# Kernel tuning notes

Hardware: AMD Instinct MI355X
Metric: run time of the kernel (lower is better)

## Reference

```python
import jax, jax.numpy as jnp
import numpy as np

N = 2048
E = 32768
H = 128
EDGE_FEAT_DIM = 4


def _mlp(x, w1, b1, w2, b2):
    return jax.nn.relu(x @ w1 + b1) @ w2 + b2


def setup_inputs() -> dict:
    key = jax.random.key(0)
    ks = jax.random.split(key, 20)
    s = 0.02
    inp = {
        "mu": jax.random.normal(ks[0], (N, H), jnp.float32),
        "sigma": jax.random.uniform(ks[1], (N, H), jnp.float32),
        "edge_index": jax.random.randint(ks[2], (2, E), 0, N, jnp.int32),
        "edge_dist": jax.random.uniform(ks[3], (E, 1), jnp.float32),
        "edge_conf": jax.random.uniform(ks[4], (E, 1), jnp.float32),
        "edge_angle": jax.random.normal(ks[5], (E, 1), jnp.float32),
        "edge_depth_diff": jax.random.normal(ks[6], (E, 1), jnp.float32),
        # msg_mlp: (2H+4 -> H -> H)
        "msg_w1": jax.random.normal(ks[7], (2 * H + EDGE_FEAT_DIM, H), jnp.float32) * s,
        "msg_b1": jnp.zeros((H,), jnp.float32),
        "msg_w2": jax.random.normal(ks[8], (H, H), jnp.float32) * s,
        "msg_b2": jnp.zeros((H,), jnp.float32),
        # mu_update_mlp: (H -> H -> H)
        "mu_w1": jax.random.normal(ks[9], (H, H), jnp.float32) * s,
        "mu_b1": jnp.zeros((H,), jnp.float32),
        "mu_w2": jax.random.normal(ks[10], (H, H), jnp.float32) * s,
        "mu_b2": jnp.zeros((H,), jnp.float32),
        # sigma_update_mlp: (H+1 -> H -> H)
        "sig_w1": jax.random.normal(ks[11], (H + 1, H), jnp.float32) * s,
        "sig_b1": jnp.zeros((H,), jnp.float32),
        "sig_w2": jax.random.normal(ks[12], (H, H), jnp.float32) * s,
        "sig_b2": jnp.zeros((H,), jnp.float32),
    }
    return inp


def _residuals(edge_index, edge_dist, num_nodes):
    src, dst = edge_index[0], edge_index[1]
    d_AC = edge_dist[:, 0]                                  # (E,)
    adj = jnp.full((num_nodes, num_nodes), -1.0, edge_dist.dtype)
    adj = adj.at[src, dst].set(d_AC)                        # (N, N)
    d_AB = adj[src]                                         # (E, N): d(A, B)
    d_BC_T = adj[:, dst].T                                  # (E, N): d(B, C)
    valid = (d_AB >= 0) & (d_BC_T >= 0)
    two_hop = jnp.where(valid, d_AB + d_BC_T, 0.0)
    path_count = valid.sum(axis=1).astype(edge_dist.dtype)  # (E,)
    mean_two_hop = jnp.where(
        path_count > 0,
        two_hop.sum(axis=1) / jnp.maximum(path_count, 1.0),
        d_AC,
    )
    return jnp.abs(d_AC - mean_two_hop)[:, None]            # (E, 1)


def reference(mu, sigma, edge_index, edge_dist, edge_conf, edge_angle,
              edge_depth_diff, msg_w1, msg_b1, msg_w2, msg_b2,
              mu_w1, mu_b1, mu_w2, mu_b2, sig_w1, sig_b1, sig_w2, sig_b2):
    n = mu.shape[0]
    src, dst = edge_index[0], edge_index[1]
    residuals = _residuals(edge_index, edge_dist, n)        # (E, 1)
    weights = jnp.exp(-residuals)                           # (E, 1)
    edge_feat = jnp.concatenate([edge_dist, edge_conf, edge_angle, edge_depth_diff], axis=-1)
    msg_input = jnp.concatenate([mu[src], sigma[src], edge_feat], axis=-1)
    messages = _mlp(msg_input, msg_w1, msg_b1, msg_w2, msg_b2)  # (E, H)
    weighted_msgs = messages * weights
    agg_msg = jax.ops.segment_sum(weighted_msgs, dst, num_segments=n)
    weight_sum = jax.ops.segment_sum(weights, dst, num_segments=n)
    agg_msg = agg_msg / jnp.maximum(weight_sum, 1e-8)
    mu_new = mu + _mlp(agg_msg, mu_w1, mu_b1, mu_w2, mu_b2)
    # scatter-mean of residuals over incoming edges
    r_sum = jax.ops.segment_sum(residuals, dst, num_segments=n)
    cnt = jax.ops.segment_sum(jnp.ones((residuals.shape[0], 1), residuals.dtype), dst, num_segments=n)
    mean_incoming_r = r_sum / jnp.maximum(cnt, 1.0)
    sigma_input = jnp.concatenate([agg_msg, mean_incoming_r], axis=-1)
    sigma_new = jax.nn.softplus(_mlp(sigma_input, sig_w1, sig_b1, sig_w2, sig_b2))
    return mu_new, sigma_new, residuals
```

## Files before the change

kernel.cpp:

```cpp
#include <hip/hip_runtime.h>
#include <math.h>

#define NNODE 2048
#define NEDGE 32768
#define HID   128
#define NMAT  (NNODE * NNODE)
#define EB    64

__global__ __launch_bounds__(256) void init_kernel(int4* __restrict__ adj4,
                                                   int* __restrict__ deg_src,
                                                   int* __restrict__ deg_dst) {
    int gid = blockIdx.x * 256 + threadIdx.x;
    adj4[gid] = make_int4(-1, -1, -1, -1);
    if (gid < NNODE) { deg_src[gid] = 0; deg_dst[gid] = 0; }
}

__global__ __launch_bounds__(256) void scatter_kernel(const int* __restrict__ ei,
                                                      int* __restrict__ adj_idx,
                                                      int* __restrict__ deg_src,
                                                      int* __restrict__ deg_dst) {
    int e = blockIdx.x * 256 + threadIdx.x;
    if (e < NEDGE) {
        int s = ei[e];
        int d = ei[NEDGE + e];
        atomicMax(&adj_idx[(size_t)s * NNODE + d], e);
        atomicAdd(&deg_src[s], 1);
        atomicAdd(&deg_dst[d], 1);
    }
}

__global__ __launch_bounds__(256) void scan_kernel(const int* __restrict__ deg_src,
                                                   const int* __restrict__ deg_dst,
                                                   int* __restrict__ off_src,
                                                   int* __restrict__ off_dst,
                                                   int* __restrict__ cur_src,
                                                   int* __restrict__ cur_dst) {
    __shared__ int part[256];
    int t = threadIdx.x;
    for (int which = 0; which < 2; ++which) {
        const int* deg = which ? deg_dst : deg_src;
        int* off = which ? off_dst : off_src;
        int* cur = which ? cur_dst : cur_src;
        __syncthreads();
        int base = t * 8;
        int local[8];
        int s = 0;
        #pragma unroll
        for (int i = 0; i < 8; ++i) { local[i] = deg[base + i]; s += local[i]; }
        part[t] = s;
        __syncthreads();
        if (t == 0) {
            int run = 0;
            for (int i = 0; i < 256; ++i) { int v = part[i]; part[i] = run; run += v; }
        }
        __syncthreads();
        int run = part[t];
        #pragma unroll
        for (int i = 0; i < 8; ++i) {
            off[base + i] = run;
            cur[base + i] = run;
            run += local[i];
        }
        if (t == 255) off[NNODE] = run;
    }
}

__global__ __launch_bounds__(256) void fill_kernel(const int* __restrict__ ei,
                                                   int* __restrict__ cur_src,
                                                   int* __restrict__ cur_dst,
                                                   int* __restrict__ list_src,
                                                   int* __restrict__ list_dst) {
    int e = blockIdx.x * 256 + threadIdx.x;
    if (e < NEDGE) {
        int s = ei[e];
        int d = ei[NEDGE + e];
        int p1 = atomicAdd(&cur_src[s], 1);
        list_src[p1] = e;
        int p2 = atomicAdd(&cur_dst[d], 1);
        list_dst[p2] = e;
    }
}

__global__ __launch_bounds__(256) void residual_kernel(const int* __restrict__ ei,
                                                       const float* __restrict__ dist,
                                                       const int* __restrict__ adj_idx,
                                                       const int* __restrict__ off_src,
                                                       const int* __restrict__ list_src,
                                                       float* __restrict__ res_out,
                                                       float* __restrict__ wbuf) {
    int grp = threadIdx.x >> 4;
    int lane = threadIdx.x & 15;
    int e = blockIdx.x * 16 + grp;
    int A = ei[e];
    int C = ei[NEDGE + e];
    int beg = off_src[A];
    int end = off_src[A + 1];
    float sum = 0.0f, cnt = 0.0f;
    for (int i = beg + lane; i < end; i += 16) {
        int ep = list_src[i];
        int B = ei[NEDGE + ep];
        if (adj_idx[(size_t)A * NNODE + B] == ep) {
            int idx2 = adj_idx[(size_t)B * NNODE + C];
            if (idx2 >= 0) { sum += dist[ep] + dist[idx2]; cnt += 1.0f; }
        }
    }
    #pragma unroll
    for (int off = 8; off > 0; off >>= 1) {
        sum += __shfl_down(sum, off, 16);
        cnt += __shfl_down(cnt, off, 16);
    }
    if (lane == 0) {
        float d = dist[e];
        float mean = (cnt > 0.0f) ? (sum / cnt) : d;
        float r = fabsf(d - mean);
        res_out[e] = r;
        wbuf[e] = expf(-r);
    }
}

__global__ __launch_bounds__(256) void node_part_kernel(const float* __restrict__ mu,
                                                        const float* __restrict__ sigma,
                                                        const float* __restrict__ w1,
                                                        const float* __restrict__ b1,
                                                        float* __restrict__ np) {
    __shared__ float xs[16][35];
    __shared__ float wt[32 * HID];
    int tid = threadIdx.x;
    int n0 = blockIdx.x * 16;
    int nl = tid & 15, jg = tid >> 4, j0 = jg * 8;
    float acc[8];
    #pragma unroll
    for (int r = 0; r < 8; ++r) acc[r] = b1[j0 + r];
    for (int t = 0; t < 8; ++t) {
        const float* src = (t < 4) ? mu : sigma;
        int kbase = (t < 4) ? t * 32 : (t - 4) * 32;
        __syncthreads();
        if (tid < 128) {
            int row = tid >> 3, c4 = (tid & 7) << 2;
            float4 v = *(const float4*)(src + (size_t)(n0 + row) * HID + kbase + c4);
            xs[row][c4] = v.x; xs[row][c4 + 1] = v.y;
            xs[row][c4 + 2] = v.z; xs[row][c4 + 3] = v.w;
        }
        {
            const float4* wsrc = (const float4*)(w1 + (size_t)(t * 32) * HID);
            for (int i = tid; i < 32 * (HID / 4); i += 256) ((float4*)wt)[i] = wsrc[i];
        }
        __syncthreads();
        #pragma unroll 2
        for (int kk = 0; kk < 32; ++kk) {
            float xv = xs[nl][kk];
            const float* wr = wt + kk * HID + j0;
            #pragma unroll
            for (int r = 0; r < 8; ++r) acc[r] = fmaf(xv, wr[r], acc[r]);
        }
    }
    float* orow = np + (size_t)(n0 + nl) * HID + j0;
    *(float4*)orow = make_float4(acc[0], acc[1], acc[2], acc[3]);
    *(float4*)(orow + 4) = make_float4(acc[4], acc[5], acc[6], acc[7]);
}

__global__ __launch_bounds__(256, 4) void msg_kernel(const float* __restrict__ np,
                                                     const int* __restrict__ ei,
                                                     const float* __restrict__ dist,
                                                     const float* __restrict__ conf,
                                                     const float* __restrict__ angle,
                                                     const float* __restrict__ ddiff,
                                                     const float* __restrict__ w1,
                                                     const float* __restrict__ w2,
                                                     const float* __restrict__ b2,
                                                     float* __restrict__ wmsg) {
    __shared__ float hs[EB][131];
    __shared__ float wt[32 * HID];
    __shared__ float w1c[4][HID];
    __shared__ int   sid[EB];
    __shared__ float sef[4][EB];
    int tid = threadIdx.x;
    int e0 = blockIdx.x * EB;
    if (tid < EB) {
        int ge = e0 + tid;
        sid[tid] = ei[ge];
        sef[0][tid] = dist[ge];
        sef[1][tid] = conf[ge];
        sef[2][tid] = angle[ge];
        sef[3][tid] = ddiff[ge];
    }
    for (int i = tid; i < 4 * HID; i += 256)
        w1c[i >> 7][i & 127] = w1[(size_t)(2 * HID) * HID + i];
    __syncthreads();

    int eg = tid & 15, jg = tid >> 4, j0 = jg * 8;

    #pragma unroll
    for (int q = 0; q < 4; ++q) {
        int el = 4 * eg + q;
        const float* nrow = np + (size_t)sid[el] * HID + j0;
        float4 a = *(const float4*)nrow;
        float4 b = *(const float4*)(nrow + 4);
        float f0 = sef[0][el], f1 = sef[1][el], f2 = sef[2][el], f3 = sef[3][el];
        float base[8] = {a.x, a.y, a.z, a.w, b.x, b.y, b.z, b.w};
        #pragma unroll
        for (int r = 0; r < 8; ++r) {
            float v = base[r];
            v = fmaf(f0, w1c[0][j0 + r], v);
            v = fmaf(f1, w1c[1][j0 + r], v);
            v = fmaf(f2, w1c[2][j0 + r], v);
            v = fmaf(f3, w1c[3][j0 + r], v);
            hs[el][j0 + r] = fmaxf(v, 0.0f);
        }
    }

    float acc[4][8];
    #pragma unroll
    for (int q = 0; q < 4; ++q)
        #pragma unroll
        for (int r = 0; r < 8; ++r) acc[q][r] = b2[j0 + r];
    for (int t = 0; t < 4; ++t) {
        int k0 = t * 32;
        __syncthreads();
        {
            const float4* src = (const float4*)(w2 + (size_t)k0 * HID);
            for (int i = tid; i < 32 * (HID / 4); i += 256) ((float4*)wt)[i] = src[i];
        }
        __syncthreads();
        #pragma unroll 2
        for (int kk = 0; kk < 32; ++kk) {
            float4 wa = *(const float4*)&wt[kk * HID + j0];
            float4 wb = *(const float4*)&wt[kk * HID + j0 + 4];
            #pragma unroll
            for (int q = 0; q < 4; ++q) {
                float xv = hs[4 * eg + q][k0 + kk];
                acc[q][0] = fmaf(xv, wa.x, acc[q][0]);
                acc[q][1] = fmaf(xv, wa.y, acc[q][1]);
                acc[q][2] = fmaf(xv, wa.z, acc[q][2]);
                acc[q][3] = fmaf(xv, wa.w, acc[q][3]);
                acc[q][4] = fmaf(xv, wb.x, acc[q][4]);
                acc[q][5] = fmaf(xv, wb.y, acc[q][5]);
                acc[q][6] = fmaf(xv, wb.z, acc[q][6]);
                acc[q][7] = fmaf(xv, wb.w, acc[q][7]);
            }
        }
    }
    #pragma unroll
    for (int q = 0; q < 4; ++q) {
        float* orow = wmsg + (size_t)(e0 + 4 * eg + q) * HID + j0;
        *(float4*)orow = make_float4(acc[q][0], acc[q][1], acc[q][2], acc[q][3]);
        *(float4*)(orow + 4) = make_float4(acc[q][4], acc[q][5], acc[q][6], acc[q][7]);
    }
}

__global__ __launch_bounds__(128) void gather_kernel(const float* __restrict__ wmsg,
                                                     const float* __restrict__ wbuf,
                                                     const float* __restrict__ res,
                                                     const int* __restrict__ off_dst,
                                                     const int* __restrict__ list_dst,
                                                     float* __restrict__ aggn,
                                                     float* __restrict__ mean_r) {
    int n = blockIdx.x;
    int j = threadIdx.x;
    int beg = off_dst[n];
    int end = off_dst[n + 1];
    float acc = 0.0f, ws = 0.0f, rs = 0.0f;
    for (int i = beg; i < end; ++i) {
        int e = list_dst[i];
        float w = wbuf[e];
        acc += w * wmsg[(size_t)e * HID + j];
        ws += w;
        rs += res[e];
    }
    aggn[(size_t)n * HID + j] = acc / fmaxf(ws, 1e-8f);
    if (j == 0) {
        float c = (float)(end - beg);
        mean_r[n] = rs / fmaxf(c, 1.0f);
    }
}

__global__ __launch_bounds__(256) void node_out_kernel(const float* __restrict__ mu,
                                                       const float* __restrict__ aggn,
                                                       const float* __restrict__ mean_r,
                                                       const float* __restrict__ mu_w1,
                                                       const float* __restrict__ mu_b1,
                                                       const float* __restrict__ mu_w2,
                                                       const float* __restrict__ mu_b2,
                                                       const float* __restrict__ sg_w1,
                                                       const float* __restrict__ sg_b1,
                                                       const float* __restrict__ sg_w2,
                                                       const float* __restrict__ sg_b2,
                                                       float* __restrict__ out_mu,
                                                       float* __restrict__ out_sig) {
    __shared__ float xs[16][133];
    __shared__ float wt[32 * HID];
    __shared__ float hs[16][131];
    bool is_mu = blockIdx.x < (NNODE / 16);
    int bi = is_mu ? blockIdx.x : blockIdx.x - NNODE / 16;
    int n0 = bi * 16;
    const float* w1 = is_mu ? mu_w1 : sg_w1;
    const float* b1 = is_mu ? mu_b1 : sg_b1;
    const float* w2 = is_mu ? mu_w2 : sg_w2;
    const float* b2 = is_mu ? mu_b2 : sg_b2;
    int K1 = is_mu ? HID : (HID + 1);
    int tid = threadIdx.x;
    int nl = tid & 15, jg = tid >> 4, j0 = jg * 8;
    for (int i = tid; i < 512; i += 256) {
        int row = i >> 5, c4 = (i & 31) * 4;
        float4 v = *(const float4*)(aggn + (size_t)(n0 + row) * HID + c4);
        xs[row][c4] = v.x; xs[row][c4 + 1] = v.y;
        xs[row][c4 + 2] = v.z; xs[row][c4 + 3] = v.w;
    }
    if (!is_mu && tid < 16) xs[tid][HID] = mean_r[n0 + tid];
    float acc[8];
    #pragma unroll
    for (int r = 0; r < 8; ++r) acc[r] = b1[j0 + r];
    for (int k0 = 0; k0 < K1; k0 += 32) {
        int rows = (K1 - k0 < 32) ? (K1 - k0) : 32;
        __syncthreads();
        {
            const float4* src = (const float4*)(w1 + (size_t)k0 * HID);
            for (int i = tid; i < rows * (HID / 4); i += 256) ((float4*)wt)[i] = src[i];
        }
        __syncthreads();
        #pragma unroll 2
        for (int kk = 0; kk < rows; ++kk) {
            float xv = xs[nl][k0 + kk];
            const float* wr = wt + kk * HID + j0;
            #pragma unroll
            for (int r = 0; r < 8; ++r) acc[r] = fmaf(xv, wr[r], acc[r]);
        }
    }
    #pragma unroll
    for (int r = 0; r < 8; ++r) hs[nl][j0 + r] = fmaxf(acc[r], 0.0f);
    #pragma unroll
    for (int r = 0; r < 8; ++r) acc[r] = b2[j0 + r];
    for (int k0 = 0; k0 < HID; k0 += 32) {
        __syncthreads();
        {
            const float4* src = (const float4*)(w2 + (size_t)k0 * HID);
            for (int i = tid; i < 32 * (HID / 4); i += 256) ((float4*)wt)[i] = src[i];
        }
        __syncthreads();
        #pragma unroll 2
        for (int kk = 0; kk < 32; ++kk) {
            float xv = hs[nl][k0 + kk];
            const float* wr = wt + kk * HID + j0;
            #pragma unroll
            for (int r = 0; r < 8; ++r) acc[r] = fmaf(xv, wr[r], acc[r]);
        }
    }
    int n = n0 + nl;
    if (is_mu) {
        #pragma unroll
        for (int r = 0; r < 8; ++r)
            out_mu[(size_t)n * HID + j0 + r] = mu[(size_t)n * HID + j0 + r] + acc[r];
    } else {
        #pragma unroll
        for (int r = 0; r < 8; ++r) {
            float x = acc[r];
            out_sig[(size_t)n * HID + j0 + r] = fmaxf(x, 0.0f) + log1pf(expf(-fabsf(x)));
        }
    }
}

extern "C" void kernel_launch(void* const* d_in, const int* in_sizes, int n_in,
                              void* d_out, int out_size, void* d_ws, size_t ws_size,
                              hipStream_t stream) {
    const float* mu     = (const float*)d_in[0];
    const float* sigma  = (const float*)d_in[1];
    const int*   ei     = (const int*)d_in[2];
    const float* dist   = (const float*)d_in[3];
    const float* conf   = (const float*)d_in[4];
    const float* angle  = (const float*)d_in[5];
    const float* ddiff  = (const float*)d_in[6];
    const float* msg_w1 = (const float*)d_in[7];
    const float* msg_b1 = (const float*)d_in[8];
    const float* msg_w2 = (const float*)d_in[9];
    const float* msg_b2 = (const float*)d_in[10];
    const float* mu_w1  = (const float*)d_in[11];
    const float* mu_b1  = (const float*)d_in[12];
    const float* mu_w2  = (const float*)d_in[13];
    const float* mu_b2  = (const float*)d_in[14];
    const float* sig_w1 = (const float*)d_in[15];
    const float* sig_b1 = (const float*)d_in[16];
    const float* sig_w2 = (const float*)d_in[17];
    const float* sig_b2 = (const float*)d_in[18];

    float* out_mu  = (float*)d_out;
    float* out_sig = out_mu + (size_t)NNODE * HID;
    float* out_res = out_sig + (size_t)NNODE * HID;

    char* ws = (char*)d_ws;
    size_t o = 0;
    int*   adj_idx  = (int*)(ws + o);   o += (size_t)NMAT * 4;
    float* wmsg     = (float*)(ws + o); o += (size_t)NEDGE * HID * 4;
    float* wbuf     = (float*)(ws + o); o += (size_t)NEDGE * 4;
    float* aggn     = (float*)(ws + o); o += (size_t)NNODE * HID * 4;
    float* mean_r   = (float*)(ws + o); o += (size_t)NNODE * 4;
    int*   deg_src  = (int*)(ws + o);   o += (size_t)NNODE * 4;
    int*   deg_dst  = (int*)(ws + o);   o += (size_t)NNODE * 4;
    int*   off_src  = (int*)(ws + o);   o += (size_t)(NNODE + 1) * 4;
    int*   off_dst  = (int*)(ws + o);   o += (size_t)(NNODE + 1) * 4;
    int*   cur_src  = (int*)(ws + o);   o += (size_t)NNODE * 4;
    int*   cur_dst  = (int*)(ws + o);   o += (size_t)NNODE * 4;
    int*   list_src = (int*)(ws + o);   o += (size_t)NEDGE * 4;
    int*   list_dst = (int*)(ws + o);   o += (size_t)NEDGE * 4;
    float* np = aggn;

    hipLaunchKernelGGL(init_kernel, dim3(4096), dim3(256), 0, stream,
                       (int4*)adj_idx, deg_src, deg_dst);
    hipLaunchKernelGGL(scatter_kernel, dim3(NEDGE / 256), dim3(256), 0, stream,
                       ei, adj_idx, deg_src, deg_dst);
    hipLaunchKernelGGL(scan_kernel, dim3(1), dim3(256), 0, stream,
                       deg_src, deg_dst, off_src, off_dst, cur_src, cur_dst);
    hipLaunchKernelGGL(fill_kernel, dim3(NEDGE / 256), dim3(256), 0, stream,
                       ei, cur_src, cur_dst, list_src, list_dst);
    hipLaunchKernelGGL(residual_kernel, dim3(NEDGE / 16), dim3(256), 0, stream,
                       ei, dist, adj_idx, off_src, list_src, out_res, wbuf);
    hipLaunchKernelGGL(node_part_kernel, dim3(NNODE / 16), dim3(256), 0, stream,
                       mu, sigma, msg_w1, msg_b1, np);
    hipLaunchKernelGGL(msg_kernel, dim3(NEDGE / EB), dim3(256), 0, stream,
                       np, ei, dist, conf, angle, ddiff,
                       msg_w1, msg_w2, msg_b2, wmsg);
    hipLaunchKernelGGL(gather_kernel, dim3(NNODE), dim3(128), 0, stream,
                       wmsg, wbuf, out_res, off_dst, list_dst, aggn, mean_r);
    hipLaunchKernelGGL(node_out_kernel, dim3(2 * (NNODE / 16)), dim3(256), 0, stream,
                       mu, aggn, mean_r,
                       mu_w1, mu_b1, mu_w2, mu_b2,
                       sig_w1, sig_b1, sig_w2, sig_b2,
                       out_mu, out_sig);
}
```

Baseline: 216.2 us.

## Fuse residual into message kernel and write messages in dst-sorted order

Folds the separate residual kernel into the message kernel, with 4 lanes per edge. Messages, weights and residuals are written directly to dst-sorted slots, so the gather kernel reads contiguous rows instead of going through list_dst. The degree histogram moves into the single-block scan kernel using shared-memory atomics, and the serial scan is replaced by a wavefront shuffle scan. The gather kernel now handles two nodes per block. This cuts kernel launches and indirect gather reads, but the fused residual loop may add imbalance to the message kernel, and the single-block histogram serializes 64K atomics.

```diff
diff --git a/kernel.cpp b/kernel.cpp
--- a/kernel.cpp
+++ b/kernel.cpp
@@ -7,61 +7,62 @@
 #define NMAT  (NNODE * NNODE)
 #define EB    64
 
-__global__ __launch_bounds__(256) void init_kernel(int4* __restrict__ adj4,
-                                                   int* __restrict__ deg_src,
-                                                   int* __restrict__ deg_dst) {
+__global__ __launch_bounds__(256) void init_kernel(int4* __restrict__ adj4) {
     int gid = blockIdx.x * 256 + threadIdx.x;
     adj4[gid] = make_int4(-1, -1, -1, -1);
-    if (gid < NNODE) { deg_src[gid] = 0; deg_dst[gid] = 0; }
 }
 
 __global__ __launch_bounds__(256) void scatter_kernel(const int* __restrict__ ei,
-                                                      int* __restrict__ adj_idx,
-                                                      int* __restrict__ deg_src,
-                                                      int* __restrict__ deg_dst) {
+                                                      int* __restrict__ adj_idx) {
     int e = blockIdx.x * 256 + threadIdx.x;
     if (e < NEDGE) {
         int s = ei[e];
         int d = ei[NEDGE + e];
         atomicMax(&adj_idx[(size_t)s * NNODE + d], e);
-        atomicAdd(&deg_src[s], 1);
-        atomicAdd(&deg_dst[d], 1);
-    }
-}
-
-__global__ __launch_bounds__(256) void scan_kernel(const int* __restrict__ deg_src,
-                                                   const int* __restrict__ deg_dst,
-                                                   int* __restrict__ off_src,
-                                                   int* __restrict__ off_dst,
-                                                   int* __restrict__ cur_src,
-                                                   int* __restrict__ cur_dst) {
-    __shared__ int part[256];
+    }
+}
+
+__global__ __launch_bounds__(256) void scan_hist_kernel(const int* __restrict__ ei,
+                                                        int* __restrict__ off_src,
+                                                        int* __restrict__ off_dst,
+                                                        int* __restrict__ cur_src,
+                                                        int* __restrict__ cur_dst) {
+    __shared__ int hist[NNODE];
+    __shared__ int wsum[4];
     int t = threadIdx.x;
     for (int which = 0; which < 2; ++which) {
-        const int* deg = which ? deg_dst : deg_src;
+        const int* idx = ei + (which ? NEDGE : 0);
         int* off = which ? off_dst : off_src;
         int* cur = which ? cur_dst : cur_src;
+        for (int i = t; i < NNODE; i += 256) hist[i] = 0;
+        __syncthreads();
+        for (int i = t; i < NEDGE; i += 256) atomicAdd(&hist[idx[i]], 1);
         __syncthreads();
         int base = t * 8;
         int local[8];
         int s = 0;
         #pragma unroll
-        for (int i = 0; i < 8; ++i) { local[i] = deg[base + i]; s += local[i]; }
-        part[t] = s;
-        __syncthreads();
-        if (t == 0) {
-            int run = 0;
-            for (int i = 0; i < 256; ++i) { int v = part[i]; part[i] = run; run += v; }
-        }
-        __syncthreads();
-        int run = part[t];
+        for (int i = 0; i < 8; ++i) { local[i] = hist[base + i]; s += local[i]; }
+        int lane = t & 63, w = t >> 6;
+        int run = s;
+        #pragma unroll
+        for (int d = 1; d < 64; d <<= 1) {
+            int v = __shfl_up(run, d, 64);
+            if (lane >= d) run += v;
+        }
+        if (lane == 63) wsum[w] = run;
+        __syncthreads();
+        int wbase = 0;
+        for (int i = 0; i < w; ++i) wbase += wsum[i];
+        int excl = wbase + run - s;
         #pragma unroll
         for (int i = 0; i < 8; ++i) {
-            off[base + i] = run;
-            cur[base + i] = run;
-            run += local[i];
-        }
-        if (t == 255) off[NNODE] = run;
+            off[base + i] = excl;
+            cur[base + i] = excl;
+            excl += local[i];
+        }
+        if (t == 255) off[NNODE] = excl;
+        __syncthreads();
     }
 }
 
@@ -69,7 +70,7 @@
                                                    int* __restrict__ cur_src,
                                                    int* __restrict__ cur_dst,
                                                    int* __restrict__ list_src,
-                                                   int* __restrict__ list_dst) {
+                                                   int* __restrict__ slot_dst) {
     int e = blockIdx.x * 256 + threadIdx.x;
     if (e < NEDGE) {
         int s = ei[e];
@@ -77,44 +78,7 @@
         int p1 = atomicAdd(&cur_src[s], 1);
         list_src[p1] = e;
         int p2 = atomicAdd(&cur_dst[d], 1);
-        list_dst[p2] = e;
-    }
-}
-
-__global__ __launch_bounds__(256) void residual_kernel(const int* __restrict__ ei,
-                                                       const float* __restrict__ dist,
-                                                       const int* __restrict__ adj_idx,
-                                                       const int* __restrict__ off_src,
-                                                       const int* __restrict__ list_src,
-                                                       float* __restrict__ res_out,
-                                                       float* __restrict__ wbuf) {
-    int grp = threadIdx.x >> 4;
-    int lane = threadIdx.x & 15;
-    int e = blockIdx.x * 16 + grp;
-    int A = ei[e];
-    int C = ei[NEDGE + e];
-    int beg = off_src[A];
-    int end = off_src[A + 1];
-    float sum = 0.0f, cnt = 0.0f;
-    for (int i = beg + lane; i < end; i += 16) {
-        int ep = list_src[i];
-        int B = ei[NEDGE + ep];
-        if (adj_idx[(size_t)A * NNODE + B] == ep) {
-            int idx2 = adj_idx[(size_t)B * NNODE + C];
-            if (idx2 >= 0) { sum += dist[ep] + dist[idx2]; cnt += 1.0f; }
-        }
-    }
-    #pragma unroll
-    for (int off = 8; off > 0; off >>= 1) {
-        sum += __shfl_down(sum, off, 16);
-        cnt += __shfl_down(cnt, off, 16);
-    }
-    if (lane == 0) {
-        float d = dist[e];
-        float mean = (cnt > 0.0f) ? (sum / cnt) : d;
-        float r = fabsf(d - mean);
-        res_out[e] = r;
-        wbuf[e] = expf(-r);
+        slot_dst[e] = p2;
     }
 }
 
@@ -159,26 +123,37 @@
     *(float4*)(orow + 4) = make_float4(acc[4], acc[5], acc[6], acc[7]);
 }
 
-__global__ __launch_bounds__(256, 4) void msg_kernel(const float* __restrict__ np,
-                                                     const int* __restrict__ ei,
-                                                     const float* __restrict__ dist,
-                                                     const float* __restrict__ conf,
-                                                     const float* __restrict__ angle,
-                                                     const float* __restrict__ ddiff,
-                                                     const float* __restrict__ w1,
-                                                     const float* __restrict__ w2,
-                                                     const float* __restrict__ b2,
-                                                     float* __restrict__ wmsg) {
+__global__ __launch_bounds__(256, 4) void msgres_kernel(const float* __restrict__ np,
+                                                        const int* __restrict__ ei,
+                                                        const float* __restrict__ dist,
+                                                        const float* __restrict__ conf,
+                                                        const float* __restrict__ angle,
+                                                        const float* __restrict__ ddiff,
+                                                        const int* __restrict__ adj_idx,
+                                                        const int* __restrict__ off_src,
+                                                        const int* __restrict__ list_src,
+                                                        const int* __restrict__ slot_dst,
+                                                        const float* __restrict__ w1,
+                                                        const float* __restrict__ w2,
+                                                        const float* __restrict__ b2,
+                                                        float* __restrict__ out_res,
+                                                        float* __restrict__ wsort,
+                                                        float* __restrict__ rsort,
+                                                        float* __restrict__ wmsg) {
     __shared__ float hs[EB][131];
     __shared__ float wt[32 * HID];
     __shared__ float w1c[4][HID];
     __shared__ int   sid[EB];
+    __shared__ int   sdt[EB];
+    __shared__ int   sslot[EB];
     __shared__ float sef[4][EB];
     int tid = threadIdx.x;
     int e0 = blockIdx.x * EB;
     if (tid < EB) {
         int ge = e0 + tid;
         sid[tid] = ei[ge];
+        sdt[tid] = ei[NEDGE + ge];
+        sslot[tid] = slot_dst[ge];
         sef[0][tid] = dist[ge];
         sef[1][tid] = conf[ge];
         sef[2][tid] = angle[ge];
@@ -187,6 +162,32 @@
     for (int i = tid; i < 4 * HID; i += 256)
         w1c[i >> 7][i & 127] = w1[(size_t)(2 * HID) * HID + i];
     __syncthreads();
+
+    {
+        int el = tid >> 2, li = tid & 3;
+        int A = sid[el], C = sdt[el];
+        int beg = off_src[A], end = off_src[A + 1];
+        float sum = 0.0f, cnt = 0.0f;
+        for (int i = beg + li; i < end; i += 4) {
+            int ep = list_src[i];
+            int B = ei[NEDGE + ep];
+            if (adj_idx[(size_t)A * NNODE + B] == ep) {
+                int idx2 = adj_idx[(size_t)B * NNODE + C];
+                if (idx2 >= 0) { sum += dist[ep] + dist[idx2]; cnt += 1.0f; }
+            }
+        }
+        sum += __shfl_xor(sum, 1, 4); cnt += __shfl_xor(cnt, 1, 4);
+        sum += __shfl_xor(sum, 2, 4); cnt += __shfl_xor(cnt, 2, 4);
+        if (li == 0) {
+            float d = sef[0][el];
+            float mean = (cnt > 0.0f) ? (sum / cnt) : d;
+            float r = fabsf(d - mean);
+            out_res[e0 + el] = r;
+            int slot = sslot[el];
+            wsort[slot] = expf(-r);
+            rsort[slot] = r;
+        }
+    }
 
     int eg = tid & 15, jg = tid >> 4, j0 = jg * 8;
 
@@ -242,30 +243,28 @@
     }
     #pragma unroll
     for (int q = 0; q < 4; ++q) {
-        float* orow = wmsg + (size_t)(e0 + 4 * eg + q) * HID + j0;
+        float* orow = wmsg + (size_t)sslot[4 * eg + q] * HID + j0;
         *(float4*)orow = make_float4(acc[q][0], acc[q][1], acc[q][2], acc[q][3]);
         *(float4*)(orow + 4) = make_float4(acc[q][4], acc[q][5], acc[q][6], acc[q][7]);
     }
 }
 
-__global__ __launch_bounds__(128) void gather_kernel(const float* __restrict__ wmsg,
-                                                     const float* __restrict__ wbuf,
-                                                     const float* __restrict__ res,
+__global__ __launch_bounds__(256) void gather_kernel(const float* __restrict__ wmsg,
+                                                     const float* __restrict__ wsort,
+                                                     const float* __restrict__ rsort,
                                                      const int* __restrict__ off_dst,
-                                                     const int* __restrict__ list_dst,
                                                      float* __restrict__ aggn,
                                                      float* __restrict__ mean_r) {
-    int n = blockIdx.x;
-    int j = threadIdx.x;
+    int n = blockIdx.x * 2 + (threadIdx.x >> 7);
+    int j = threadIdx.x & 127;
     int beg = off_dst[n];
     int end = off_dst[n + 1];
     float acc = 0.0f, ws = 0.0f, rs = 0.0f;
     for (int i = beg; i < end; ++i) {
-        int e = list_dst[i];
-        float w = wbuf[e];
-        acc += w * wmsg[(size_t)e * HID + j];
+        float w = wsort[i];
+        acc += w * wmsg[(size_t)i * HID + j];
         ws += w;
-        rs += res[e];
+        rs += rsort[i];
     }
     aggn[(size_t)n * HID + j] = acc / fmaxf(ws, 1e-8f);
     if (j == 0) {
@@ -390,36 +389,35 @@
     size_t o = 0;
     int*   adj_idx  = (int*)(ws + o);   o += (size_t)NMAT * 4;
     float* wmsg     = (float*)(ws + o); o += (size_t)NEDGE * HID * 4;
-    float* wbuf     = (float*)(ws + o); o += (size_t)NEDGE * 4;
+    float* wsort    = (float*)(ws + o); o += (size_t)NEDGE * 4;
+    float* rsort    = (float*)(ws + o); o += (size_t)NEDGE * 4;
     float* aggn     = (float*)(ws + o); o += (size_t)NNODE * HID * 4;
     float* mean_r   = (float*)(ws + o); o += (size_t)NNODE * 4;
-    int*   deg_src  = (int*)(ws + o);   o += (size_t)NNODE * 4;
-    int*   deg_dst  = (int*)(ws + o);   o += (size_t)NNODE * 4;
     int*   off_src  = (int*)(ws + o);   o += (size_t)(NNODE + 1) * 4;
     int*   off_dst  = (int*)(ws + o);   o += (size_t)(NNODE + 1) * 4;
     int*   cur_src  = (int*)(ws + o);   o += (size_t)NNODE * 4;
     int*   cur_dst  = (int*)(ws + o);   o += (size_t)NNODE * 4;
     int*   list_src = (int*)(ws + o);   o += (size_t)NEDGE * 4;
-    int*   list_dst = (int*)(ws + o);   o += (size_t)NEDGE * 4;
+    int*   slot_dst = (int*)(ws + o);   o += (size_t)NEDGE * 4;
     float* np = aggn;
 
     hipLaunchKernelGGL(init_kernel, dim3(4096), dim3(256), 0, stream,
-                       (int4*)adj_idx, deg_src, deg_dst);
+                       (int4*)adj_idx);
     hipLaunchKernelGGL(scatter_kernel, dim3(NEDGE / 256), dim3(256), 0, stream,
-                       ei, adj_idx, deg_src, deg_dst);
-    hipLaunchKernelGGL(scan_kernel, dim3(1), dim3(256), 0, stream,
-                       deg_src, deg_dst, off_src, off_dst, cur_src, cur_dst);
+                       ei, adj_idx);
+    hipLaunchKernelGGL(scan_hist_kernel, dim3(1), dim3(256), 0, stream,
+                       ei, off_src, off_dst, cur_src, cur_dst);
     hipLaunchKernelGGL(fill_kernel, dim3(NEDGE / 256), dim3(256), 0, stream,
-                       ei, cur_src, cur_dst, list_src, list_dst);
-    hipLaunchKernelGGL(residual_kernel, dim3(NEDGE / 16), dim3(256), 0, stream,
-                       ei, dist, adj_idx, off_src, list_src, out_res, wbuf);
+                       ei, cur_src, cur_dst, list_src, slot_dst);
     hipLaunchKernelGGL(node_part_kernel, dim3(NNODE / 16), dim3(256), 0, stream,
                        mu, sigma, msg_w1, msg_b1, np);
-    hipLaunchKernelGGL(msg_kernel, dim3(NEDGE / EB), dim3(256), 0, stream,
+    hipLaunchKernelGGL(msgres_kernel, dim3(NEDGE / EB), dim3(256), 0, stream,
                        np, ei, dist, conf, angle, ddiff,
-                       msg_w1, msg_w2, msg_b2, wmsg);
-    hipLaunchKernelGGL(gather_kernel, dim3(NNODE), dim3(128), 0, stream,
-                       wmsg, wbuf, out_res, off_dst, list_dst, aggn, mean_r);
+                       adj_idx, off_src, list_src, slot_dst,
+                       msg_w1, msg_w2, msg_b2,
+                       out_res, wsort, rsort, wmsg);
+    hipLaunchKernelGGL(gather_kernel, dim3(NNODE / 2), dim3(256), 0, stream,
+                       wmsg, wsort, rsort, off_dst, aggn, mean_r);
     hipLaunchKernelGGL(node_out_kernel, dim3(2 * (NNODE / 16)), dim3(256), 0, stream,
                        mu, aggn, mean_r,
                        mu_w1, mu_b1, mu_w2, mu_b2,
```

Result: slower. 263.0 us (+21.6%).
